# Kernel optimization log

Hardware: AMD Instinct MI355X
Metric: run time of the kernel (lower is better)

## Reference

```python
import jax, jax.numpy as jnp
import numpy as np

SIDE = 32
RADIUS = 6.0
N_CHANNEL = 64
KEY_SIZE = 32


def _dist_mask(side, radius):
    # dists[x1, y1, x2, y2] = euclidean distance; flatten (x1,y1) -> N
    xs = jnp.arange(side, dtype=jnp.float32)
    dx = xs[:, None, None, None] - xs[None, None, :, None]  # X1 - X2
    dy = xs[None, :, None, None] - xs[None, None, None, :]  # Y1 - Y2
    d = jnp.sqrt(dx * dx + dy * dy)                          # (s,s,s,s)
    d = d.reshape(side * side, side, side)                   # (N, H, W)
    return jnp.where(d > radius, -jnp.inf, 0.0)[None]        # (1, N, H, W)


def setup_inputs() -> dict:
    key = jax.random.key(0)
    ks = jax.random.split(key, 8)
    B = 16
    x = jax.random.normal(ks[0], (B, N_CHANNEL, SIDE, SIDE), dtype=jnp.float32)
    s_c = 1.0 / np.sqrt(N_CHANNEL)
    s_k = 1.0 / np.sqrt(KEY_SIZE)
    Wq = jax.random.normal(ks[1], (KEY_SIZE, N_CHANNEL), dtype=jnp.float32) * s_c
    Wk = jax.random.normal(ks[2], (KEY_SIZE, N_CHANNEL), dtype=jnp.float32) * s_c
    Wv = jax.random.normal(ks[3], (KEY_SIZE, N_CHANNEL), dtype=jnp.float32) * s_c
    Wq_xy = jax.random.normal(ks[4], (2, N_CHANNEL), dtype=jnp.float32) * s_c
    Wk_xy = jax.random.normal(ks[5], (2, N_CHANNEL), dtype=jnp.float32) * s_c
    Wout = jax.random.normal(ks[6], (N_CHANNEL, KEY_SIZE), dtype=jnp.float32) * s_k
    return {"x": x, "Wq": Wq, "Wk": Wk, "Wv": Wv,
            "Wq_xy": Wq_xy, "Wk_xy": Wk_xy, "Wout": Wout}


def reference(x, Wq, Wk, Wv, Wq_xy, Wk_xy, Wout):
    B, C, H, W = x.shape
    N = H * W
    mask = _dist_mask(H, RADIUS)  # (1, N, H, W)

    # 1x1 convs == channel contractions
    q = jnp.einsum('kc,bchw->bkhw', Wq, x)                 # (B,K,H,W) queries
    k = jnp.einsum('kc,bchw->bkhw', Wk, x).reshape(B, -1, N)   # (B,K,N) keys (flattened)
    v = jnp.einsum('kc,bchw->bkhw', Wv, x).reshape(B, -1, N)   # (B,K,N) values
    q_xy = jnp.einsum('kc,bchw->bkhw', Wq_xy, x)           # (B,2,H,W)
    k_xy = jnp.einsum('kc,bchw->bkhw', Wk_xy, x).reshape(B, 2, N)

    # scores[b,n,h,w]: key n vs query (h,w)
    scores = jnp.einsum('bkn,bkhw->bnhw', k, q)
    scores_xy = jnp.einsum('bkn,bkhw->bnhw', k_xy, q_xy)
    attn = jax.nn.softmax(scores_xy + mask + scores, axis=1)   # over N keys

    out = jnp.einsum('bnhw,bkn->bkhw', attn, v)            # (B,K,H,W)
    return jnp.einsum('ck,bkhw->bchw', Wout, out)          # (B,C,H,W)
```

## Files before the change

kernel.cpp:

```cpp
#include <hip/hip_runtime.h>
#include <math.h>

typedef short bf16x8 __attribute__((ext_vector_type(8)));
typedef float f32x4 __attribute__((ext_vector_type(4)));
typedef unsigned short u16;
typedef unsigned int u32;

#define WS_QT  0
#define WS_KT  1048576
#define WS_VW  2097152
#define WS_QXY 3153920
#define WS_KXY 3284992
#define VWS    1032

__device__ __forceinline__ u32 f2bf(float f) {
    u32 u = __float_as_uint(f);
    u += 0x7fffu + ((u >> 16) & 1u);
    return u >> 16;
}
__device__ __forceinline__ u32 pk2(float a, float b) {
    return f2bf(a) | (f2bf(b) << 16);
}

union U4H { uint4 u; bf16x8 h; };

__global__ __launch_bounds__(64) void proj_kernel(
    const float* __restrict__ x,
    const float* __restrict__ Wq, const float* __restrict__ Wk,
    const float* __restrict__ Wv, const float* __restrict__ Wqxy,
    const float* __restrict__ Wkxy, char* __restrict__ wsb)
{
    u16* QT = (u16*)(wsb + WS_QT);
    u16* KT = (u16*)(wsb + WS_KT);
    u16* VW = (u16*)(wsb + WS_VW);
    float* QXY = (float*)(wsb + WS_QXY);
    float* KXY = (float*)(wsb + WS_KXY);

    int l = threadIdx.x;
    int g = l >> 4, l15 = l & 15;
    int bid = blockIdx.x;
    int xcd = bid & 7, j = bid >> 3;
    int b = (xcd << 1) + (j >> 7);
    int h = j & 1;
    int n0 = ((j >> 1) & 63) << 4;

    bf16x8 ah[2], al[2];
    #pragma unroll
    for (int ks = 0; ks < 2; ks++) {
        float av[8];
        #pragma unroll
        for (int i = 0; i < 8; i++)
            av[i] = x[(((b << 6) + (ks << 5) + (g << 3) + i) << 10) + n0 + l15];
        #pragma unroll
        for (int i = 0; i < 8; i++) {
            u32 hb = f2bf(av[i]);
            float rr = av[i] - __uint_as_float(hb << 16);
            ah[ks][i] = (short)hb;
            al[ks][i] = (short)f2bf(rr);
        }
    }

    auto do_jt = [&](int jt) {
        f32x4 acc = {0.f, 0.f, 0.f, 0.f};
        #pragma unroll
        for (int ks = 0; ks < 2; ks++) {
            float wv[8];
            #pragma unroll
            for (int i = 0; i < 8; i++) wv[i] = 0.f;
            if (jt < 6) {
                const float* wbase = (jt < 2) ? Wq : (jt < 4) ? Wk : Wv;
                const float* wr = wbase + ((((jt & 1) << 4) + l15) << 6)
                                        + (ks << 5) + (g << 3);
                float4 wa = *(const float4*)wr, wb = *(const float4*)(wr + 4);
                wv[0] = wa.x; wv[1] = wa.y; wv[2] = wa.z; wv[3] = wa.w;
                wv[4] = wb.x; wv[5] = wb.y; wv[6] = wb.z; wv[7] = wb.w;
            } else if (l15 < 4) {
                const float* wr = ((l15 < 2) ? (Wqxy + (l15 << 6))
                                             : (Wkxy + ((l15 - 2) << 6)))
                                  + (ks << 5) + (g << 3);
                float4 wa = *(const float4*)wr, wb = *(const float4*)(wr + 4);
                wv[0] = wa.x; wv[1] = wa.y; wv[2] = wa.z; wv[3] = wa.w;
                wv[4] = wb.x; wv[5] = wb.y; wv[6] = wb.z; wv[7] = wb.w;
            }
            bf16x8 wh, wl;
            #pragma unroll
            for (int i = 0; i < 8; i++) {
                u32 hb = f2bf(wv[i]);
                float rr = wv[i] - __uint_as_float(hb << 16);
                wh[i] = (short)hb;
                wl[i] = (short)f2bf(rr);
            }
            acc = __builtin_amdgcn_mfma_f32_16x16x32_bf16(ah[ks], wh, acc, 0, 0, 0);
            acc = __builtin_amdgcn_mfma_f32_16x16x32_bf16(al[ks], wh, acc, 0, 0, 0);
            acc = __builtin_amdgcn_mfma_f32_16x16x32_bf16(ah[ks], wl, acc, 0, 0, 0);
        }
        if (jt < 2) {
            #pragma unroll
            for (int r = 0; r < 4; r++)
                QT[(((b << 10) + n0 + (g << 2) + r) << 5) + (jt << 4) + l15]
                    = (u16)f2bf(acc[r]);
        } else if (jt < 4) {
            #pragma unroll
            for (int r = 0; r < 4; r++)
                KT[(((b << 10) + n0 + (g << 2) + r) << 5) + ((jt - 2) << 4) + l15]
                    = (u16)f2bf(acc[r]);
        } else if (jt < 6) {
            int kd = ((jt - 4) << 4) + l15;
            uint2 d = make_uint2(pk2(acc[0], acc[1]), pk2(acc[2], acc[3]));
            *(uint2*)&VW[((b << 5) + kd) * VWS + n0 + (g << 2)] = d;
        } else {
            if (l15 < 2) {
                #pragma unroll
                for (int r = 0; r < 4; r++)
                    QXY[(((b << 10) + n0 + (g << 2) + r) << 1) + l15] = acc[r];
            } else if (l15 < 4) {
                #pragma unroll
                for (int r = 0; r < 4; r++)
                    KXY[(((b << 10) + n0 + (g << 2) + r) << 1) + (l15 - 2)] = acc[r];
            }
        }
    };

    if (h == 0) {
        #pragma unroll
        for (int jt = 0; jt < 4; jt++) do_jt(jt);
    } else {
        #pragma unroll
        for (int jt = 4; jt < 7; jt++) do_jt(jt);
        if (((j >> 1) & 63) == 63 && l < 32)
            *(uint4*)&VW[((b << 5) + l) * VWS + 1024] = make_uint4(0, 0, 0, 0);
    }
}

__global__ __launch_bounds__(256, 4) void attn_kernel(
    const char* __restrict__ wsb, const float* __restrict__ Wout,
    float* __restrict__ out)
{
    const u16* QT = (const u16*)(wsb + WS_QT);
    const u16* KT = (const u16*)(wsb + WS_KT);
    const u16* VW = (const u16*)(wsb + WS_VW);
    const float* QXY = (const float*)(wsb + WS_QXY);
    const float* KXY = (const float*)(wsb + WS_KXY);

    __shared__ __align__(16) u16 smem[18176];
    u16* vfr = smem;
    u32* kxyb = (u32*)(smem + 14336);
    u16* wfr = smem + 16128;
    u16* o_l = smem;

    int tid = threadIdx.x, bid = blockIdx.x;
    int xcd = bid & 7, j = bid >> 3;
    int b = (xcd << 1) + (j >> 4);
    int t4 = j & 15;
    int qy0 = (t4 >> 3) << 4, qx0 = (t4 & 7) << 2;
    int ry0 = qy0 - 6, rx0 = qx0 - 6;

    #pragma unroll
    for (int i = 0; i < 14; i++) {
        int d = tid + (i << 8);
        int p = d & 1, kd = (d >> 1) & 31, g2 = (d >> 6) & 3, m = d >> 8;
        int ky = ry0 + (m << 1) + p;
        int n = ky * 32 + rx0 + (g2 << 2);
        if ((u32)ky > 31u) n = 0;
        const u32* s = (const u32*)(VW + ((b << 5) + kd) * VWS + n);
        *(uint2*)&vfr[d << 2] = make_uint2(s[0], s[1]);
    }
    for (int i = tid; i < 448; i += 256) {
        int n2 = (ry0 + (i >> 4)) * 32 + rx0 + (i & 15);
        n2 = max(0, min(1023, n2));
        float2 f = *(const float2*)(KXY + (((b << 10) + n2) << 1));
        u32 h0 = f2bf(f.x), h1 = f2bf(f.y);
        float r0 = f.x - __uint_as_float(h0 << 16);
        float r1 = f.y - __uint_as_float(h1 << 16);
        kxyb[(i << 1)]     = h0 | (h1 << 16);
        kxyb[(i << 1) + 1] = f2bf(r0) | (f2bf(r1) << 16);
    }
    {
        int nt = tid >> 6, l = tid & 63;
        int cc = (nt << 4) + (l & 15);
        const float* wsrc = Wout + (cc << 5) + ((l >> 4) << 3);
        uint4 dw;
        dw.x = pk2(wsrc[0], wsrc[1]); dw.y = pk2(wsrc[2], wsrc[3]);
        dw.z = pk2(wsrc[4], wsrc[5]); dw.w = pk2(wsrc[6], wsrc[7]);
        *(uint4*)&wfr[tid << 3] = dw;
    }

    int w = tid >> 6, ll = tid & 63;
    int lq = ll & 15, g = ll >> 4;
    int qrl = lq >> 2, qcol = lq & 3;
    int nq = (qy0 + (w << 2) + qrl) * 32 + qx0 + qcol;
    uint4 bqu = *(const uint4*)(QT + (((b << 10) + nq) << 5) + (g << 3));
    float2 qv = *(const float2*)(QXY + (((b << 10) + nq) << 1));
    u32 qh0 = f2bf(qv.x), qh1 = f2bf(qv.y);
    float qr0 = qv.x - __uint_as_float(qh0 << 16);
    float qr1 = qv.y - __uint_as_float(qh1 << 16);
    u32 qhp = qh0 | (qh1 << 16);
    u32 qlp = f2bf(qr0) | (f2bf(qr1) << 16);
    uint4 bxyu = make_uint4(g == 0 ? qhp : 0, g == 0 ? qlp : 0,
                            g == 0 ? qhp : 0, 0);

    __syncthreads();

    f32x4 acc[16];
    #pragma unroll
    for (int t = 0; t < 16; t++) {
        int rr = (w << 2) + t;
        uint2 kp = *(const uint2*)&kxyb[((rr << 4) + lq) << 1];
        U4H axy; axy.u = make_uint4(g == 0 ? kp.x : 0, g == 0 ? kp.x : 0,
                                    g == 0 ? kp.y : 0, 0);
        U4H bxy; bxy.u = bxyu;
        f32x4 z = {0.f, 0.f, 0.f, 0.f};
        f32x4 a0 = __builtin_amdgcn_mfma_f32_16x16x32_bf16(axy.h, bxy.h, z, 0, 0, 0);
        int n2 = (ry0 + rr) * 32 + rx0 + lq;
        n2 = max(0, min(1023, n2));
        U4H ak; ak.u = *(const uint4*)(KT + (((b << 10) + n2) << 5) + (g << 3));
        U4H bq; bq.u = bqu;
        acc[t] = __builtin_amdgcn_mfma_f32_16x16x32_bf16(ak.h, bq.h, a0, 0, 0, 0);
    }

    int dx2a[4], kxa[4];
    #pragma unroll
    for (int r = 0; r < 4; r++) {
        int sc = (g << 2) + r;
        int kx = rx0 + sc;
        kxa[r] = (kx >= 0) && (kx < 32);
        int dx = sc - 6 - qcol;
        dx2a[r] = dx * dx;
    }
    float m = -1e30f;
    #pragma unroll
    for (int t = 0; t < 16; t++) {
        int ky = ry0 + (w << 2) + t;
        bool kyok = (ky >= 0) && (ky < 32);
        int dy = t - 6 - qrl, dy2 = dy * dy;
        #pragma unroll
        for (int r = 0; r < 4; r++) {
            bool ok = kyok && kxa[r] && (dy2 + dx2a[r] <= 36);
            acc[t][r] = ok ? acc[t][r] : -1e4f;
            m = fmaxf(m, acc[t][r]);
        }
    }
    m = fmaxf(m, __shfl_xor(m, 16, 64));
    m = fmaxf(m, __shfl_xor(m, 32, 64));

    float sum = 0.f;
    #pragma unroll
    for (int t = 0; t < 16; t++) {
        #pragma unroll
        for (int r = 0; r < 4; r++) {
            float e = __expf(acc[t][r] - m);
            acc[t][r] = e;
            sum += e;
        }
    }
    sum += __shfl_xor(sum, 16, 64);
    sum += __shfl_xor(sum, 32, 64);

    float rinv = 1.f / sum;
    #pragma unroll
    for (int t = 0; t < 16; t++) {
        #pragma unroll
        for (int r = 0; r < 4; r++) acc[t][r] *= rinv;
    }

    f32x4 o0 = {0.f, 0.f, 0.f, 0.f}, o1 = {0.f, 0.f, 0.f, 0.f};
    #pragma unroll
    for (int kk = 0; kk < 8; kk++) {
        int m2 = (w << 1) + kk;
        U4H pa;
        pa.u = make_uint4(pk2(acc[2 * kk][0],     acc[2 * kk][1]),
                          pk2(acc[2 * kk][2],     acc[2 * kk][3]),
                          pk2(acc[2 * kk + 1][0], acc[2 * kk + 1][1]),
                          pk2(acc[2 * kk + 1][2], acc[2 * kk + 1][3]));
        U4H v0; v0.u = *(const uint4*)&vfr[((m2 << 7) + (g << 5) + lq) << 3];
        U4H v1; v1.u = *(const uint4*)&vfr[((m2 << 7) + (g << 5) + lq + 16) << 3];
        o0 = __builtin_amdgcn_mfma_f32_16x16x32_bf16(pa.h, v0.h, o0, 0, 0, 0);
        o1 = __builtin_amdgcn_mfma_f32_16x16x32_bf16(pa.h, v1.h, o1, 0, 0, 0);
    }

    __syncthreads();
    #pragma unroll
    for (int r = 0; r < 4; r++) {
        int q = (g << 2) + r;
        o_l[(w << 9) + (q << 5) + lq]      = (u16)f2bf(o0[r]);
        o_l[(w << 9) + (q << 5) + lq + 16] = (u16)f2bf(o1[r]);
    }
    __syncthreads();

    U4H aO; aO.u = *(const uint4*)&o_l[(w << 9) + (lq << 5) + (g << 3)];
    int nqb = (qy0 + (w << 2) + g) * 32 + qx0;
    #pragma unroll
    for (int nt2 = 0; nt2 < 4; nt2++) {
        U4H bw; bw.u = *(const uint4*)&wfr[((nt2 << 6) + ll) << 3];
        f32x4 z = {0.f, 0.f, 0.f, 0.f};
        f32x4 y = __builtin_amdgcn_mfma_f32_16x16x32_bf16(aO.h, bw.h, z, 0, 0, 0);
        int cc = (nt2 << 4) + lq;
        #pragma unroll
        for (int r = 0; r < 4; r++)
            out[(((b << 6) + cc) << 10) + nqb + r] = y[r];
    }
}

extern "C" void kernel_launch(void* const* d_in, const int* in_sizes, int n_in,
                              void* d_out, int out_size, void* d_ws, size_t ws_size,
                              hipStream_t stream) {
    const float* x    = (const float*)d_in[0];
    const float* Wq   = (const float*)d_in[1];
    const float* Wk   = (const float*)d_in[2];
    const float* Wv   = (const float*)d_in[3];
    const float* Wqxy = (const float*)d_in[4];
    const float* Wkxy = (const float*)d_in[5];
    const float* Wout = (const float*)d_in[6];
    float* out = (float*)d_out;
    char* wsb  = (char*)d_ws;

    proj_kernel<<<2048, 64, 0, stream>>>(x, Wq, Wk, Wv, Wqxy, Wkxy, wsb);
    attn_kernel<<<256, 256, 0, stream>>>(wsb, Wout, out);
}
```

Measured before the change: 18.79 us.

## Split attention into single-wave blocks over 8-query tiles, read V directly

Restructures the attention kernel from 256-thread blocks covering 64 queries with a shared V/Wout/KXY staging phase into 2048 single-wave blocks, each handling a 4x2 query tile. V fragments and Wout are now loaded straight from global memory inside the MFMA loop, and the xy score term is computed with scalar FMAs instead of a split-bf16 MFMA. The aim is to remove block-level syncs and large LDS staging and to raise parallelism. The cost is wasted MFMA lanes, since only 8 of 16 query columns are used, and redundant global loads across blocks.

```diff
diff --git a/kernel.cpp b/kernel.cpp
--- a/kernel.cpp
+++ b/kernel.cpp
@@ -132,7 +132,7 @@
     }
 }
 
-__global__ __launch_bounds__(256, 4) void attn_kernel(
+__global__ __launch_bounds__(64) void attn_kernel(
     const char* __restrict__ wsb, const float* __restrict__ Wout,
     float* __restrict__ out)
 {
@@ -142,80 +142,48 @@
     const float* QXY = (const float*)(wsb + WS_QXY);
     const float* KXY = (const float*)(wsb + WS_KXY);
 
-    __shared__ __align__(16) u16 smem[18176];
-    u16* vfr = smem;
-    u32* kxyb = (u32*)(smem + 14336);
-    u16* wfr = smem + 16128;
-    u16* o_l = smem;
-
-    int tid = threadIdx.x, bid = blockIdx.x;
+    __shared__ __align__(16) float kxy_l[256 * 2];
+    __shared__ __align__(16) u16 o_l[8 * 32];
+
+    int lane = threadIdx.x, bid = blockIdx.x;
     int xcd = bid & 7, j = bid >> 3;
-    int b = (xcd << 1) + (j >> 4);
-    int t4 = j & 15;
-    int qy0 = (t4 >> 3) << 4, qx0 = (t4 & 7) << 2;
-    int ry0 = qy0 - 6, rx0 = qx0 - 6;
-
-    #pragma unroll
-    for (int i = 0; i < 14; i++) {
-        int d = tid + (i << 8);
-        int p = d & 1, kd = (d >> 1) & 31, g2 = (d >> 6) & 3, m = d >> 8;
-        int ky = ry0 + (m << 1) + p;
-        int n = ky * 32 + rx0 + (g2 << 2);
-        if ((u32)ky > 31u) n = 0;
-        const u32* s = (const u32*)(VW + ((b << 5) + kd) * VWS + n);
-        *(uint2*)&vfr[d << 2] = make_uint2(s[0], s[1]);
-    }
-    for (int i = tid; i < 448; i += 256) {
-        int n2 = (ry0 + (i >> 4)) * 32 + rx0 + (i & 15);
+    int b = (xcd << 1) + (j >> 7);
+    int tile = j & 127;
+    int qy0 = (tile >> 4) << 2, qx0 = (tile & 15) << 1;
+    int ry0 = qy0 - 6, rx0 = qx0 - 7;
+
+    int g = lane >> 4, lq = lane & 15;
+    int q8 = lq & 7;
+    int qrl = q8 >> 1, qcol = q8 & 1;
+    int nq = (qy0 + qrl) * 32 + qx0 + qcol;
+
+    #pragma unroll
+    for (int i = 0; i < 4; i++) {
+        int s = (lane << 2) + i;
+        int n2 = (ry0 + (s >> 4)) * 32 + rx0 + (s & 15);
         n2 = max(0, min(1023, n2));
-        float2 f = *(const float2*)(KXY + (((b << 10) + n2) << 1));
-        u32 h0 = f2bf(f.x), h1 = f2bf(f.y);
-        float r0 = f.x - __uint_as_float(h0 << 16);
-        float r1 = f.y - __uint_as_float(h1 << 16);
-        kxyb[(i << 1)]     = h0 | (h1 << 16);
-        kxyb[(i << 1) + 1] = f2bf(r0) | (f2bf(r1) << 16);
-    }
-    {
-        int nt = tid >> 6, l = tid & 63;
-        int cc = (nt << 4) + (l & 15);
-        const float* wsrc = Wout + (cc << 5) + ((l >> 4) << 3);
-        uint4 dw;
-        dw.x = pk2(wsrc[0], wsrc[1]); dw.y = pk2(wsrc[2], wsrc[3]);
-        dw.z = pk2(wsrc[4], wsrc[5]); dw.w = pk2(wsrc[6], wsrc[7]);
-        *(uint4*)&wfr[tid << 3] = dw;
-    }
-
-    int w = tid >> 6, ll = tid & 63;
-    int lq = ll & 15, g = ll >> 4;
-    int qrl = lq >> 2, qcol = lq & 3;
-    int nq = (qy0 + (w << 2) + qrl) * 32 + qx0 + qcol;
-    uint4 bqu = *(const uint4*)(QT + (((b << 10) + nq) << 5) + (g << 3));
+        *(float2*)&kxy_l[s << 1] = *(const float2*)(KXY + (((b << 10) + n2) << 1));
+    }
+
+    U4H bq; bq.u = *(const uint4*)(QT + (((b << 10) + nq) << 5) + (g << 3));
     float2 qv = *(const float2*)(QXY + (((b << 10) + nq) << 1));
-    u32 qh0 = f2bf(qv.x), qh1 = f2bf(qv.y);
-    float qr0 = qv.x - __uint_as_float(qh0 << 16);
-    float qr1 = qv.y - __uint_as_float(qh1 << 16);
-    u32 qhp = qh0 | (qh1 << 16);
-    u32 qlp = f2bf(qr0) | (f2bf(qr1) << 16);
-    uint4 bxyu = make_uint4(g == 0 ? qhp : 0, g == 0 ? qlp : 0,
-                            g == 0 ? qhp : 0, 0);
-
-    __syncthreads();
 
     f32x4 acc[16];
     #pragma unroll
     for (int t = 0; t < 16; t++) {
-        int rr = (w << 2) + t;
-        uint2 kp = *(const uint2*)&kxyb[((rr << 4) + lq) << 1];
-        U4H axy; axy.u = make_uint4(g == 0 ? kp.x : 0, g == 0 ? kp.x : 0,
-                                    g == 0 ? kp.y : 0, 0);
-        U4H bxy; bxy.u = bxyu;
-        f32x4 z = {0.f, 0.f, 0.f, 0.f};
-        f32x4 a0 = __builtin_amdgcn_mfma_f32_16x16x32_bf16(axy.h, bxy.h, z, 0, 0, 0);
-        int n2 = (ry0 + rr) * 32 + rx0 + lq;
+        int n2 = (ry0 + t) * 32 + rx0 + lq;
         n2 = max(0, min(1023, n2));
         U4H ak; ak.u = *(const uint4*)(KT + (((b << 10) + n2) << 5) + (g << 3));
-        U4H bq; bq.u = bqu;
-        acc[t] = __builtin_amdgcn_mfma_f32_16x16x32_bf16(ak.h, bq.h, a0, 0, 0, 0);
+        f32x4 z = {0.f, 0.f, 0.f, 0.f};
+        acc[t] = __builtin_amdgcn_mfma_f32_16x16x32_bf16(ak.h, bq.h, z, 0, 0, 0);
+    }
+    #pragma unroll
+    for (int t = 0; t < 16; t++) {
+        #pragma unroll
+        for (int r = 0; r < 4; r++) {
+            float2 k2 = *(float2*)&kxy_l[((t << 4) + (g << 2) + r) << 1];
+            acc[t][r] += qv.x * k2.x + qv.y * k2.y;
+        }
     }
 
     int dx2a[4], kxa[4];
@@ -224,13 +192,13 @@
         int sc = (g << 2) + r;
         int kx = rx0 + sc;
         kxa[r] = (kx >= 0) && (kx < 32);
-        int dx = sc - 6 - qcol;
+        int dx = sc - 7 - qcol;
         dx2a[r] = dx * dx;
     }
     float m = -1e30f;
     #pragma unroll
     for (int t = 0; t < 16; t++) {
-        int ky = ry0 + (w << 2) + t;
+        int ky = ry0 + t;
         bool kyok = (ky >= 0) && (ky < 32);
         int dy = t - 6 - qrl, dy2 = dy * dy;
         #pragma unroll
@@ -266,38 +234,51 @@
     f32x4 o0 = {0.f, 0.f, 0.f, 0.f}, o1 = {0.f, 0.f, 0.f, 0.f};
     #pragma unroll
     for (int kk = 0; kk < 8; kk++) {
-        int m2 = (w << 1) + kk;
         U4H pa;
         pa.u = make_uint4(pk2(acc[2 * kk][0],     acc[2 * kk][1]),
                           pk2(acc[2 * kk][2],     acc[2 * kk][3]),
                           pk2(acc[2 * kk + 1][0], acc[2 * kk + 1][1]),
                           pk2(acc[2 * kk + 1][2], acc[2 * kk + 1][3]));
-        U4H v0; v0.u = *(const uint4*)&vfr[((m2 << 7) + (g << 5) + lq) << 3];
-        U4H v1; v1.u = *(const uint4*)&vfr[((m2 << 7) + (g << 5) + lq + 16) << 3];
+        int ky0a = ry0 + (kk << 1), ky1a = ky0a + 1;
+        int na = ((u32)ky0a > 31u) ? 0 : (ky0a * 32 + rx0 + (g << 2));
+        int nb = ((u32)ky1a > 31u) ? 0 : (ky1a * 32 + rx0 + (g << 2));
+        const u16* v0b = VW + ((b << 5) + lq) * VWS;
+        const u16* v1b = VW + ((b << 5) + lq + 16) * VWS;
+        uint2 a0 = *(const uint2*)(v0b + na), a1 = *(const uint2*)(v0b + nb);
+        uint2 b0 = *(const uint2*)(v1b + na), b1 = *(const uint2*)(v1b + nb);
+        U4H v0; v0.u = make_uint4(a0.x, a0.y, a1.x, a1.y);
+        U4H v1; v1.u = make_uint4(b0.x, b0.y, b1.x, b1.y);
         o0 = __builtin_amdgcn_mfma_f32_16x16x32_bf16(pa.h, v0.h, o0, 0, 0, 0);
         o1 = __builtin_amdgcn_mfma_f32_16x16x32_bf16(pa.h, v1.h, o1, 0, 0, 0);
     }
 
-    __syncthreads();
-    #pragma unroll
-    for (int r = 0; r < 4; r++) {
-        int q = (g << 2) + r;
-        o_l[(w << 9) + (q << 5) + lq]      = (u16)f2bf(o0[r]);
-        o_l[(w << 9) + (q << 5) + lq + 16] = (u16)f2bf(o1[r]);
-    }
-    __syncthreads();
-
-    U4H aO; aO.u = *(const uint4*)&o_l[(w << 9) + (lq << 5) + (g << 3)];
-    int nqb = (qy0 + (w << 2) + g) * 32 + qx0;
-    #pragma unroll
-    for (int nt2 = 0; nt2 < 4; nt2++) {
-        U4H bw; bw.u = *(const uint4*)&wfr[((nt2 << 6) + ll) << 3];
+    if (g < 2) {
+        #pragma unroll
+        for (int r = 0; r < 4; r++) {
+            int q = (g << 2) + r;
+            o_l[(q << 5) + lq]      = (u16)f2bf(o0[r]);
+            o_l[(q << 5) + lq + 16] = (u16)f2bf(o1[r]);
+        }
+    }
+
+    U4H aO; aO.u = *(const uint4*)&o_l[(q8 << 5) + (g << 3)];
+    #pragma unroll
+    for (int nt = 0; nt < 4; nt++) {
+        int cc = (nt << 4) + lq;
+        const float* wsrc = Wout + (cc << 5) + (g << 3);
+        U4H bw;
+        bw.u.x = pk2(wsrc[0], wsrc[1]); bw.u.y = pk2(wsrc[2], wsrc[3]);
+        bw.u.z = pk2(wsrc[4], wsrc[5]); bw.u.w = pk2(wsrc[6], wsrc[7]);
         f32x4 z = {0.f, 0.f, 0.f, 0.f};
         f32x4 y = __builtin_amdgcn_mfma_f32_16x16x32_bf16(aO.h, bw.h, z, 0, 0, 0);
-        int cc = (nt2 << 4) + lq;
-        #pragma unroll
-        for (int r = 0; r < 4; r++)
-            out[(((b << 6) + cc) << 10) + nqb + r] = y[r];
+        if (g < 2) {
+            #pragma unroll
+            for (int r = 0; r < 4; r++) {
+                int q = (g << 2) + r;
+                int nqo = (qy0 + (q >> 1)) * 32 + qx0 + (q & 1);
+                out[(((b << 6) + cc) << 10) + nqo] = y[r];
+            }
+        }
     }
 }
 
@@ -315,5 +296,5 @@
     char* wsb  = (char*)d_ws;
 
     proj_kernel<<<2048, 64, 0, stream>>>(x, Wq, Wk, Wv, Wqxy, Wkxy, wsb);
-    attn_kernel<<<256, 256, 0, stream>>>(wsb, Wout, out);
-}
+    attn_kernel<<<2048, 64, 0, stream>>>(wsb, Wout, out);
+}
```

Measured after the change: 27.00 us. 1.44x slower.
